# Optimization experiments

Hardware: AMD Instinct MI355X
Metric: run time of the kernel (lower is better)

The kernel has to match this reference:

```python
import jax, jax.numpy as jnp
import numpy as np

MAPSIZE = 256          # nearest power of two >= 224
BITS = 8               # log2(MAPSIZE)
PAD = (MAPSIZE - 224) // 2  # 16
WIBBLEDECAY = 2.0
EPSILON = 0.128
GREY = jnp.array([0.485, 0.45, 0.406], dtype=jnp.float32)


def fog_creator(fog_vars, bsize, mapsize, wibbledecay):
    """Diamond-square fractal noise with learnable perturbations (faithful port)."""
    m = jnp.zeros((bsize, mapsize, mapsize), dtype=jnp.float32)
    step = mapsize
    wibble = 1.0
    v = 0
    while step >= 2:
        h = step // 2
        # --- fillsquares: square centers = mean of 4 corners + wibble ---
        corner = m[:, 0:mapsize:step, 0:mapsize:step]          # (B, g, g)
        acc = corner + jnp.roll(corner, -1, axis=1)
        acc = acc + jnp.roll(acc, -1, axis=2)
        m = m.at[:, h:mapsize:step, h:mapsize:step].set(acc / 4.0 + wibble * fog_vars[v])
        v += 1
        # --- filldiamonds: diamond centers = mean of 4 neighbors + wibble ---
        dr = m[:, h:mapsize:step, h:mapsize:step]
        ul = m[:, 0:mapsize:step, 0:mapsize:step]
        lt = (dr + jnp.roll(dr, 1, axis=1)) + (ul + jnp.roll(ul, -1, axis=2))
        tt = (dr + jnp.roll(dr, 1, axis=2)) + (ul + jnp.roll(ul, -1, axis=1))
        m = m.at[:, 0:mapsize:step, h:mapsize:step].set(lt / 4.0 + wibble * fog_vars[v])
        v += 1
        m = m.at[:, h:mapsize:step, 0:mapsize:step].set(tt / 4.0 + wibble * fog_vars[v])
        v += 1
        step //= 2
        wibble /= wibbledecay
    return jnp.clip(jnp.abs(m), 0.0, 1.0)[:, None, :, :]  # (B, 1, M, M)


def apply_fog(inputs, fog):
    return inputs * (1.0 - fog) + fog * GREY.reshape(1, 3, 1, 1)


def setup_inputs() -> dict:
    key = jax.random.key(0)
    B = 256
    keys = jax.random.split(key, 3 * BITS + 1)
    inp = {"inputs": jax.random.uniform(keys[0], (B, 3, 224, 224), dtype=jnp.float32)}
    k = 1
    for i in range(BITS):
        g = 2 ** i
        for j in range(3):
            name = f"fog_{3 * i + j:02d}"
            inp[name] = EPSILON * jax.random.uniform(keys[k], (B, g, g), dtype=jnp.float32)
            k += 1
    return inp


def reference(inputs, fog_00, fog_01, fog_02, fog_03, fog_04, fog_05, fog_06, fog_07,
              fog_08, fog_09, fog_10, fog_11, fog_12, fog_13, fog_14, fog_15, fog_16,
              fog_17, fog_18, fog_19, fog_20, fog_21, fog_22, fog_23):
    fog_vars = [fog_00, fog_01, fog_02, fog_03, fog_04, fog_05, fog_06, fog_07,
                fog_08, fog_09, fog_10, fog_11, fog_12, fog_13, fog_14, fog_15,
                fog_16, fog_17, fog_18, fog_19, fog_20, fog_21, fog_22, fog_23]
    fog = fog_creator(fog_vars, inputs.shape[0], MAPSIZE, WIBBLEDECAY)
    fog = fog[:, :, PAD:-PAD, PAD:-PAD]  # crop 256 -> 224
    return apply_fog(inputs, fog)
```

## Files before the change

### kernel.cpp

```cpp
#include <hip/hip_runtime.h>


#define MAPB 128

struct FogPtrs { const float* f[24]; };

__global__ __launch_bounds__(1024) void fog_coarse(FogPtrs fp, float* __restrict__ Cout) {
    __shared__ float Bm[MAPB * MAPB];
    const int b = blockIdx.x;
    const int t = threadIdx.x;

    float pf0[6], pf1[6], pf2[6];
    #pragma unroll
    for (int k = 0; k < 6; ++k) {
        const int nn = 1 << (2 * k);
        if (t < nn) {
            pf0[k] = fp.f[3 * k]    [(size_t)b * nn + t];
            pf1[k] = fp.f[3 * k + 1][(size_t)b * nn + t];
            pf2[k] = fp.f[3 * k + 2][(size_t)b * nn + t];
        }
    }
    float q0[4], q1[4], q2[4];
    {
        const float* __restrict__ f0 = fp.f[18] + (size_t)b * 4096;
        const float* __restrict__ f1 = fp.f[19] + (size_t)b * 4096;
        const float* __restrict__ f2 = fp.f[20] + (size_t)b * 4096;
        #pragma unroll
        for (int it = 0; it < 4; ++it) {
            q0[it] = f0[t + it * 1024];
            q1[it] = f1[t + it * 1024];
            q2[it] = f2[t + it * 1024];
        }
    }
    if (t == 0) Bm[0] = 0.0f;
    __syncthreads();

    float w = 1.0f;
    #pragma unroll
    for (int k = 0; k < 6; ++k) {
        const int n = 1 << k, mask = n - 1;
        const int S = MAPB >> k, H = S >> 1;
        const int nn = n * n;
        if (t < nn) {
            const int i = t >> k, j = t & mask;
            const int i1 = (i + 1) & mask, j1 = (j + 1) & mask;
            const float c00 = Bm[i  * S * MAPB + j  * S];
            const float c10 = Bm[i1 * S * MAPB + j  * S];
            const float c01 = Bm[i  * S * MAPB + j1 * S];
            const float c11 = Bm[i1 * S * MAPB + j1 * S];
            Bm[(i * S + H) * MAPB + j * S + H] = (c00 + c10 + c01 + c11) * 0.25f + w * pf0[k];
        }
        __syncthreads();
        if (t < nn) {
            const int i = t >> k, j = t & mask;
            const int i1 = (i + 1) & mask, j1 = (j + 1) & mask;
            const int im = (i - 1) & mask, jm = (j - 1) & mask;
            const float dij = Bm[(i  * S + H) * MAPB + j  * S + H];
            const float dmi = Bm[(im * S + H) * MAPB + j  * S + H];
            const float dmj = Bm[(i  * S + H) * MAPB + jm * S + H];
            const float c00 = Bm[i  * S * MAPB + j  * S];
            const float c01 = Bm[i  * S * MAPB + j1 * S];
            const float c10 = Bm[i1 * S * MAPB + j  * S];
            Bm[i * S * MAPB + j * S + H]   = (dij + dmi + c00 + c01) * 0.25f + w * pf1[k];
            Bm[(i * S + H) * MAPB + j * S] = (dij + dmj + c00 + c10) * 0.25f + w * pf2[k];
        }
        __syncthreads();
        w *= 0.5f;
    }
    {
        const float w6 = 0.015625f;
        #pragma unroll
        for (int it = 0; it < 4; ++it) {
            const int idx = t + it * 1024;
            const int i = idx >> 6, j = idx & 63;
            const int i1 = (i + 1) & 63, j1 = (j + 1) & 63;
            const float c00 = Bm[i  * 2 * MAPB + j  * 2];
            const float c10 = Bm[i1 * 2 * MAPB + j  * 2];
            const float c01 = Bm[i  * 2 * MAPB + j1 * 2];
            const float c11 = Bm[i1 * 2 * MAPB + j1 * 2];
            Bm[(i * 2 + 1) * MAPB + j * 2 + 1] = (c00 + c10 + c01 + c11) * 0.25f + w6 * q0[it];
        }
        __syncthreads();
        #pragma unroll
        for (int it = 0; it < 4; ++it) {
            const int idx = t + it * 1024;
            const int i = idx >> 6, j = idx & 63;
            const int i1 = (i + 1) & 63, j1 = (j + 1) & 63;
            const int im = (i - 1) & 63, jm = (j - 1) & 63;
            const float dij = Bm[(i  * 2 + 1) * MAPB + j  * 2 + 1];
            const float dmi = Bm[(im * 2 + 1) * MAPB + j  * 2 + 1];
            const float dmj = Bm[(i  * 2 + 1) * MAPB + jm * 2 + 1];
            const float c00 = Bm[i  * 2 * MAPB + j  * 2];
            const float c01 = Bm[i  * 2 * MAPB + j1 * 2];
            const float c10 = Bm[i1 * 2 * MAPB + j  * 2];
            Bm[i * 2 * MAPB + j * 2 + 1]   = (dij + dmi + c00 + c01) * 0.25f + w6 * q1[it];
            Bm[(i * 2 + 1) * MAPB + j * 2] = (dij + dmj + c00 + c10) * 0.25f + w6 * q2[it];
        }
        __syncthreads();
    }
    float4* __restrict__ dst = (float4*)(Cout + (size_t)b * (MAPB * MAPB));
    const float4* src = (const float4*)Bm;
    #pragma unroll
    for (int it = 0; it < 4; ++it) dst[t + it * 1024] = src[t + it * 1024];
}

__global__ __launch_bounds__(512) void fog_apply(
    const float* __restrict__ inp,
    const float* __restrict__ Cg,
    const float* __restrict__ f21, const float* __restrict__ f22, const float* __restrict__ f23,
    float* __restrict__ out)
{
    __shared__ __align__(16) float sC[30 * 128];
    __shared__ __align__(16) float sD[29 * 128];
    const int b  = blockIdx.y;
    const int r0 = blockIdx.x * 56;
    const int t  = threadIdx.x;
    const int ci0 = (r0 >> 1) + 7;

    const float4* __restrict__ Cb4 = (const float4*)(Cg + (size_t)b * 16384 + (size_t)ci0 * 128);
    float4* __restrict__ sC4 = (float4*)sC;
    sC4[t] = Cb4[t];
    if (t < 448) sC4[t + 512] = Cb4[t + 512];
    __syncthreads();

    const float w7 = 0.0078125f;
    const float* __restrict__ f21b = f21 + (size_t)b * 16384 + (size_t)ci0 * 128;
    for (int idx = t; idx < 29 * 128; idx += 512) {
        const int di = idx >> 7, j = idx & 127;
        const int j1 = (j + 1) & 127;
        sD[idx] = (sC[di * 128 + j] + sC[(di + 1) * 128 + j] +
                   sC[di * 128 + j1] + sC[(di + 1) * 128 + j1]) * 0.25f
                  + w7 * f21b[idx];
    }
    __syncthreads();

    const float* __restrict__ f22b = f22 + (size_t)b * 16384;
    const float* __restrict__ f23b = f23 + (size_t)b * 16384;
    for (int p = t; p < 28 * 56; p += 512) {
        const int pr = p / 56;
        const int pc = p - pr * 56;
        const int di = pr + 1;
        const int j0 = 2 * pc + 8;
        const int gi = ci0 + di;
        const float c0  = sC[di * 128 + j0];
        const float c1  = sC[di * 128 + j0 + 1];
        const float c2  = sC[di * 128 + j0 + 2];
        const float cb0 = sC[(di + 1) * 128 + j0];
        const float cb1 = sC[(di + 1) * 128 + j0 + 1];
        const float dm  = sD[di * 128 + j0 - 1];
        const float d0  = sD[di * 128 + j0];
        const float d1  = sD[di * 128 + j0 + 1];
        const float du0 = sD[(di - 1) * 128 + j0];
        const float du1 = sD[(di - 1) * 128 + j0 + 1];
        const float2 v22 = *(const float2*)(f22b + (size_t)gi * 128 + j0);
        const float2 v23 = *(const float2*)(f23b + (size_t)gi * 128 + j0);
        const float lt0 = (d0 + du0 + c0 + c1) * 0.25f + w7 * v22.x;
        const float lt1 = (d1 + du1 + c1 + c2) * 0.25f + w7 * v22.y;
        const float tt0 = (d0 + dm + c0 + cb0) * 0.25f + w7 * v23.x;
        const float tt1 = (d1 + d0 + c1 + cb1) * 0.25f + w7 * v23.y;
        const float fa = fminf(fabsf(c0),  1.0f);
        const float fb = fminf(fabsf(lt0), 1.0f);
        const float fc = fminf(fabsf(c1),  1.0f);
        const float fd = fminf(fabsf(lt1), 1.0f);
        const float fe = fminf(fabsf(tt0), 1.0f);
        const float ff = fminf(fabsf(d0),  1.0f);
        const float fg = fminf(fabsf(tt1), 1.0f);
        const float fh = fminf(fabsf(d1),  1.0f);

        const int orow = r0 + 2 * pr;
        const int ocol = 4 * pc;
        #pragma unroll
        for (int ch = 0; ch < 3; ++ch) {
            const float g = (ch == 0) ? 0.485f : ((ch == 1) ? 0.45f : 0.406f);
            const size_t base = ((size_t)(b * 3 + ch) * 224 + orow) * 224 + ocol;
            const float4 x0 = *(const float4*)(inp + base);
            const float4 x1 = *(const float4*)(inp + base + 224);
            float4 o0, o1;
            o0.x = x0.x * (1.0f - fa) + fa * g;
            o0.y = x0.y * (1.0f - fb) + fb * g;
            o0.z = x0.z * (1.0f - fc) + fc * g;
            o0.w = x0.w * (1.0f - fd) + fd * g;
            o1.x = x1.x * (1.0f - fe) + fe * g;
            o1.y = x1.y * (1.0f - ff) + ff * g;
            o1.z = x1.z * (1.0f - fg) + fg * g;
            o1.w = x1.w * (1.0f - fh) + fh * g;
            *(float4*)(out + base)       = o0;
            *(float4*)(out + base + 224) = o1;
        }
    }
}

extern "C" void kernel_launch(void* const* d_in, const int* in_sizes, int n_in,
                              void* d_out, int out_size, void* d_ws, size_t ws_size,
                              hipStream_t stream) {
    (void)in_sizes; (void)n_in; (void)out_size; (void)ws_size;
    const float* inp = (const float*)d_in[0];
    FogPtrs fp;
    for (int v = 0; v < 24; ++v) fp.f[v] = (const float*)d_in[1 + v];
    float* Cg = (float*)d_ws;

    fog_coarse<<<dim3(256), dim3(1024), 0, stream>>>(fp, Cg);
    fog_apply<<<dim3(4, 256), dim3(512), 0, stream>>>(
        inp, Cg, fp.f[21], fp.f[22], fp.f[23], (float*)d_out);
}
```

Baseline: 355.1 us.

## Fuse coarse fog generation and apply into one kernel with nontemporal stores

```diff
diff --git a/kernel.cpp b/kernel.cpp
--- a/kernel.cpp
+++ b/kernel.cpp
@@ -3,35 +3,20 @@
 
 #define MAPB 128
 
+typedef float vf4 __attribute__((ext_vector_type(4)));
+
 struct FogPtrs { const float* f[24]; };
 
-__global__ __launch_bounds__(1024) void fog_coarse(FogPtrs fp, float* __restrict__ Cout) {
+__global__ __launch_bounds__(1024, 8) void fog_fused(
+    FogPtrs fp, const float* __restrict__ inp, float* __restrict__ out)
+{
     __shared__ float Bm[MAPB * MAPB];
-    const int b = blockIdx.x;
-    const int t = threadIdx.x;
+    __shared__ float sD[29 * 128];
+    const int bx   = blockIdx.x;
+    const int b    = bx >> 1;
+    const int half = bx & 1;
+    const int t    = threadIdx.x;
 
-    float pf0[6], pf1[6], pf2[6];
-    #pragma unroll
-    for (int k = 0; k < 6; ++k) {
-        const int nn = 1 << (2 * k);
-        if (t < nn) {
-            pf0[k] = fp.f[3 * k]    [(size_t)b * nn + t];
-            pf1[k] = fp.f[3 * k + 1][(size_t)b * nn + t];
-            pf2[k] = fp.f[3 * k + 2][(size_t)b * nn + t];
-        }
-    }
-    float q0[4], q1[4], q2[4];
-    {
-        const float* __restrict__ f0 = fp.f[18] + (size_t)b * 4096;
-        const float* __restrict__ f1 = fp.f[19] + (size_t)b * 4096;
-        const float* __restrict__ f2 = fp.f[20] + (size_t)b * 4096;
-        #pragma unroll
-        for (int it = 0; it < 4; ++it) {
-            q0[it] = f0[t + it * 1024];
-            q1[it] = f1[t + it * 1024];
-            q2[it] = f2[t + it * 1024];
-        }
-    }
     if (t == 0) Bm[0] = 0.0f;
     __syncthreads();
 
@@ -48,7 +33,8 @@
             const float c10 = Bm[i1 * S * MAPB + j  * S];
             const float c01 = Bm[i  * S * MAPB + j1 * S];
             const float c11 = Bm[i1 * S * MAPB + j1 * S];
-            Bm[(i * S + H) * MAPB + j * S + H] = (c00 + c10 + c01 + c11) * 0.25f + w * pf0[k];
+            Bm[(i * S + H) * MAPB + j * S + H] =
+                (c00 + c10 + c01 + c11) * 0.25f + w * fp.f[3 * k][(size_t)b * nn + t];
         }
         __syncthreads();
         if (t < nn) {
@@ -61,14 +47,19 @@
             const float c00 = Bm[i  * S * MAPB + j  * S];
             const float c01 = Bm[i  * S * MAPB + j1 * S];
             const float c10 = Bm[i1 * S * MAPB + j  * S];
-            Bm[i * S * MAPB + j * S + H]   = (dij + dmi + c00 + c01) * 0.25f + w * pf1[k];
-            Bm[(i * S + H) * MAPB + j * S] = (dij + dmj + c00 + c10) * 0.25f + w * pf2[k];
+            Bm[i * S * MAPB + j * S + H] =
+                (dij + dmi + c00 + c01) * 0.25f + w * fp.f[3 * k + 1][(size_t)b * nn + t];
+            Bm[(i * S + H) * MAPB + j * S] =
+                (dij + dmj + c00 + c10) * 0.25f + w * fp.f[3 * k + 2][(size_t)b * nn + t];
         }
         __syncthreads();
         w *= 0.5f;
     }
     {
         const float w6 = 0.015625f;
+        const float* __restrict__ f0 = fp.f[18] + (size_t)b * 4096;
+        const float* __restrict__ f1 = fp.f[19] + (size_t)b * 4096;
+        const float* __restrict__ f2 = fp.f[20] + (size_t)b * 4096;
         #pragma unroll
         for (int it = 0; it < 4; ++it) {
             const int idx = t + it * 1024;
@@ -78,7 +69,7 @@
             const float c10 = Bm[i1 * 2 * MAPB + j  * 2];
             const float c01 = Bm[i  * 2 * MAPB + j1 * 2];
             const float c11 = Bm[i1 * 2 * MAPB + j1 * 2];
-            Bm[(i * 2 + 1) * MAPB + j * 2 + 1] = (c00 + c10 + c01 + c11) * 0.25f + w6 * q0[it];
+            Bm[(i * 2 + 1) * MAPB + j * 2 + 1] = (c00 + c10 + c01 + c11) * 0.25f + w6 * f0[idx];
         }
         __syncthreads();
         #pragma unroll
@@ -93,113 +84,91 @@
             const float c00 = Bm[i  * 2 * MAPB + j  * 2];
             const float c01 = Bm[i  * 2 * MAPB + j1 * 2];
             const float c10 = Bm[i1 * 2 * MAPB + j  * 2];
-            Bm[i * 2 * MAPB + j * 2 + 1]   = (dij + dmi + c00 + c01) * 0.25f + w6 * q1[it];
-            Bm[(i * 2 + 1) * MAPB + j * 2] = (dij + dmj + c00 + c10) * 0.25f + w6 * q2[it];
+            Bm[i * 2 * MAPB + j * 2 + 1]   = (dij + dmi + c00 + c01) * 0.25f + w6 * f1[idx];
+            Bm[(i * 2 + 1) * MAPB + j * 2] = (dij + dmj + c00 + c10) * 0.25f + w6 * f2[idx];
         }
         __syncthreads();
     }
-    float4* __restrict__ dst = (float4*)(Cout + (size_t)b * (MAPB * MAPB));
-    const float4* src = (const float4*)Bm;
-    #pragma unroll
-    for (int it = 0; it < 4; ++it) dst[t + it * 1024] = src[t + it * 1024];
-}
-
-__global__ __launch_bounds__(512) void fog_apply(
-    const float* __restrict__ inp,
-    const float* __restrict__ Cg,
-    const float* __restrict__ f21, const float* __restrict__ f22, const float* __restrict__ f23,
-    float* __restrict__ out)
-{
-    __shared__ __align__(16) float sC[30 * 128];
-    __shared__ __align__(16) float sD[29 * 128];
-    const int b  = blockIdx.y;
-    const int r0 = blockIdx.x * 56;
-    const int t  = threadIdx.x;
-    const int ci0 = (r0 >> 1) + 7;
-
-    const float4* __restrict__ Cb4 = (const float4*)(Cg + (size_t)b * 16384 + (size_t)ci0 * 128);
-    float4* __restrict__ sC4 = (float4*)sC;
-    sC4[t] = Cb4[t];
-    if (t < 448) sC4[t + 512] = Cb4[t + 512];
-    __syncthreads();
 
     const float w7 = 0.0078125f;
-    const float* __restrict__ f21b = f21 + (size_t)b * 16384 + (size_t)ci0 * 128;
-    for (int idx = t; idx < 29 * 128; idx += 512) {
-        const int di = idx >> 7, j = idx & 127;
-        const int j1 = (j + 1) & 127;
-        sD[idx] = (sC[di * 128 + j] + sC[(di + 1) * 128 + j] +
-                   sC[di * 128 + j1] + sC[(di + 1) * 128 + j1]) * 0.25f
-                  + w7 * f21b[idx];
-    }
-    __syncthreads();
+    const float* __restrict__ f21b = fp.f[21] + (size_t)b * 16384;
+    const float* __restrict__ f22b = fp.f[22] + (size_t)b * 16384;
+    const float* __restrict__ f23b = fp.f[23] + (size_t)b * 16384;
+    #pragma unroll
+    for (int c = 0; c < 2; ++c) {
+        const int r0  = half * 112 + c * 56;
+        const int ci0 = (r0 >> 1) + 7;
+        for (int idx = t; idx < 29 * 128; idx += 1024) {
+            const int di = idx >> 7, j = idx & 127;
+            const int j1 = (j + 1) & 127;
+            const int gr = ci0 + di;
+            sD[idx] = (Bm[gr * 128 + j]  + Bm[(gr + 1) * 128 + j] +
+                       Bm[gr * 128 + j1] + Bm[(gr + 1) * 128 + j1]) * 0.25f
+                      + w7 * f21b[gr * 128 + j];
+        }
+        __syncthreads();
+        for (int p = t; p < 28 * 56; p += 1024) {
+            const int pr = p / 56;
+            const int pc = p - pr * 56;
+            const int di = pr + 1;
+            const int j0 = 2 * pc + 8;
+            const int gi = ci0 + di;
+            const float c0  = Bm[gi * 128 + j0];
+            const float c1  = Bm[gi * 128 + j0 + 1];
+            const float c2  = Bm[gi * 128 + j0 + 2];
+            const float cb0 = Bm[(gi + 1) * 128 + j0];
+            const float cb1 = Bm[(gi + 1) * 128 + j0 + 1];
+            const float dm  = sD[di * 128 + j0 - 1];
+            const float d0  = sD[di * 128 + j0];
+            const float d1  = sD[di * 128 + j0 + 1];
+            const float du0 = sD[(di - 1) * 128 + j0];
+            const float du1 = sD[(di - 1) * 128 + j0 + 1];
+            const float2 v22 = *(const float2*)(f22b + (size_t)gi * 128 + j0);
+            const float2 v23 = *(const float2*)(f23b + (size_t)gi * 128 + j0);
+            const float lt0 = (d0 + du0 + c0 + c1) * 0.25f + w7 * v22.x;
+            const float lt1 = (d1 + du1 + c1 + c2) * 0.25f + w7 * v22.y;
+            const float tt0 = (d0 + dm + c0 + cb0) * 0.25f + w7 * v23.x;
+            const float tt1 = (d1 + d0 + c1 + cb1) * 0.25f + w7 * v23.y;
+            const float fa = fminf(fabsf(c0),  1.0f);
+            const float fb = fminf(fabsf(lt0), 1.0f);
+            const float fc = fminf(fabsf(c1),  1.0f);
+            const float fd = fminf(fabsf(lt1), 1.0f);
+            const float fe = fminf(fabsf(tt0), 1.0f);
+            const float ff = fminf(fabsf(d0),  1.0f);
+            const float fg = fminf(fabsf(tt1), 1.0f);
+            const float fh = fminf(fabsf(d1),  1.0f);
 
-    const float* __restrict__ f22b = f22 + (size_t)b * 16384;
-    const float* __restrict__ f23b = f23 + (size_t)b * 16384;
-    for (int p = t; p < 28 * 56; p += 512) {
-        const int pr = p / 56;
-        const int pc = p - pr * 56;
-        const int di = pr + 1;
-        const int j0 = 2 * pc + 8;
-        const int gi = ci0 + di;
-        const float c0  = sC[di * 128 + j0];
-        const float c1  = sC[di * 128 + j0 + 1];
-        const float c2  = sC[di * 128 + j0 + 2];
-        const float cb0 = sC[(di + 1) * 128 + j0];
-        const float cb1 = sC[(di + 1) * 128 + j0 + 1];
-        const float dm  = sD[di * 128 + j0 - 1];
-        const float d0  = sD[di * 128 + j0];
-        const float d1  = sD[di * 128 + j0 + 1];
-        const float du0 = sD[(di - 1) * 128 + j0];
-        const float du1 = sD[(di - 1) * 128 + j0 + 1];
-        const float2 v22 = *(const float2*)(f22b + (size_t)gi * 128 + j0);
-        const float2 v23 = *(const float2*)(f23b + (size_t)gi * 128 + j0);
-        const float lt0 = (d0 + du0 + c0 + c1) * 0.25f + w7 * v22.x;
-        const float lt1 = (d1 + du1 + c1 + c2) * 0.25f + w7 * v22.y;
-        const float tt0 = (d0 + dm + c0 + cb0) * 0.25f + w7 * v23.x;
-        const float tt1 = (d1 + d0 + c1 + cb1) * 0.25f + w7 * v23.y;
-        const float fa = fminf(fabsf(c0),  1.0f);
-        const float fb = fminf(fabsf(lt0), 1.0f);
-        const float fc = fminf(fabsf(c1),  1.0f);
-        const float fd = fminf(fabsf(lt1), 1.0f);
-        const float fe = fminf(fabsf(tt0), 1.0f);
-        const float ff = fminf(fabsf(d0),  1.0f);
-        const float fg = fminf(fabsf(tt1), 1.0f);
-        const float fh = fminf(fabsf(d1),  1.0f);
-
-        const int orow = r0 + 2 * pr;
-        const int ocol = 4 * pc;
-        #pragma unroll
-        for (int ch = 0; ch < 3; ++ch) {
-            const float g = (ch == 0) ? 0.485f : ((ch == 1) ? 0.45f : 0.406f);
-            const size_t base = ((size_t)(b * 3 + ch) * 224 + orow) * 224 + ocol;
-            const float4 x0 = *(const float4*)(inp + base);
-            const float4 x1 = *(const float4*)(inp + base + 224);
-            float4 o0, o1;
-            o0.x = x0.x * (1.0f - fa) + fa * g;
-            o0.y = x0.y * (1.0f - fb) + fb * g;
-            o0.z = x0.z * (1.0f - fc) + fc * g;
-            o0.w = x0.w * (1.0f - fd) + fd * g;
-            o1.x = x1.x * (1.0f - fe) + fe * g;
-            o1.y = x1.y * (1.0f - ff) + ff * g;
-            o1.z = x1.z * (1.0f - fg) + fg * g;
-            o1.w = x1.w * (1.0f - fh) + fh * g;
-            *(float4*)(out + base)       = o0;
-            *(float4*)(out + base + 224) = o1;
+            const int orow = r0 + 2 * pr;
+            const int ocol = 4 * pc;
+            #pragma unroll
+            for (int ch = 0; ch < 3; ++ch) {
+                const float g = (ch == 0) ? 0.485f : ((ch == 1) ? 0.45f : 0.406f);
+                const size_t base = ((size_t)(b * 3 + ch) * 224 + orow) * 224 + ocol;
+                const float4 x0 = *(const float4*)(inp + base);
+                const float4 x1 = *(const float4*)(inp + base + 224);
+                vf4 o0, o1;
+                o0.x = x0.x * (1.0f - fa) + fa * g;
+                o0.y = x0.y * (1.0f - fb) + fb * g;
+                o0.z = x0.z * (1.0f - fc) + fc * g;
+                o0.w = x0.w * (1.0f - fd) + fd * g;
+                o1.x = x1.x * (1.0f - fe) + fe * g;
+                o1.y = x1.y * (1.0f - ff) + ff * g;
+                o1.z = x1.z * (1.0f - fg) + fg * g;
+                o1.w = x1.w * (1.0f - fh) + fh * g;
+                __builtin_nontemporal_store(o0, (vf4*)(out + base));
+                __builtin_nontemporal_store(o1, (vf4*)(out + base + 224));
+            }
         }
+        __syncthreads();
     }
 }
 
 extern "C" void kernel_launch(void* const* d_in, const int* in_sizes, int n_in,
                               void* d_out, int out_size, void* d_ws, size_t ws_size,
                               hipStream_t stream) {
-    (void)in_sizes; (void)n_in; (void)out_size; (void)ws_size;
+    (void)in_sizes; (void)n_in; (void)out_size; (void)d_ws; (void)ws_size;
     const float* inp = (const float*)d_in[0];
     FogPtrs fp;
     for (int v = 0; v < 24; ++v) fp.f[v] = (const float*)d_in[1 + v];
-    float* Cg = (float*)d_ws;
-
-    fog_coarse<<<dim3(256), dim3(1024), 0, stream>>>(fp, Cg);
-    fog_apply<<<dim3(4, 256), dim3(512), 0, stream>>>(
-        inp, Cg, fp.f[21], fp.f[22], fp.f[23], (float*)d_out);
+    fog_fused<<<dim3(512), dim3(1024), 0, stream>>>(fp, inp, (float*)d_out);
 }
```

Result: slower. 363.6 us (+2.4%).
